# Kernel tuning notes

Hardware: AMD Instinct MI355X
Metric: run time of the kernel (lower is better)

## Reference

```python
import jax, jax.numpy as jnp
import numpy as np

B, S, D = 32, 200, 256          # batch, seq_len (hard-coded 200), emb_dim (hard-coded 256)
H_CLS, H_TNS, H = 2, 4, 6       # classical heads, tensor heads, total (rate=1/3, num_heads=6)
DFF, VOCAB, L, TD = 1024, 3500, 8, 2


def layer_norm(x, g, b, eps=1e-6):
    m = x.mean(-1, keepdims=True)
    v = ((x - m) ** 2).mean(-1, keepdims=True)
    return (x - m) * jax.lax.rsqrt(v + eps) * g + b


def setup_inputs() -> dict:
    key = jax.random.key(0)
    ks = jax.random.split(key, 12)
    n = jax.random.normal
    s1 = 1.0 / np.sqrt(4 + TD - 1.0)       # TNLayer RandomNormal stddev for A1/A4
    s2 = 1.0 / np.sqrt(4 + 2 * TD - 1.0)   # for A2/A3
    return {
        "tokens": jax.random.randint(ks[0], (B, S), 0, VOCAB),
        "tok_emb": n(ks[1], (VOCAB, D)) * 0.02,
        "pos_emb": n(ks[2], (S, D)) * 0.02,
        # stacked over L layers; axis 1 of size 3 is (q, k, v)
        "wqkv_w": n(ks[3], (L, 3, D, 2 * D)) * 0.05,
        "wqkv_b": jnp.zeros((L, 3, 2 * D)),
        "A1": n(ks[4], (L, 3, 4, TD, 4)) * s1,
        "A2": n(ks[5], (L, 3, 4, TD, TD, 8)) * s2,
        "A3": n(ks[6], (L, 3, 4, TD, TD, 8)) * s2,
        "A4": n(ks[7], (L, 3, 4, TD, 4)) * s1,
        "tnb": jnp.zeros((L, 3, 4 * D)),
        "out_w": n(ks[8], (L, H * D, D)) * 0.02,
        "out_b": jnp.zeros((L, D)),
        "ff1_w": n(ks[9], (L, D, DFF)) * 0.05,
        "ff1_b": jnp.zeros((L, DFF)),
        "ff2_w": n(ks[10], (L, DFF, D)) * 0.03,
        "ff2_b": jnp.zeros((L, D)),
        "ln1_g": jnp.ones((L, D)), "ln1_b": jnp.zeros((L, D)),
        "ln2_g": jnp.ones((L, D)), "ln2_b": jnp.zeros((L, D)),
    }


def bert_tensor_forward(tokens, tok_emb, pos_emb, wqkv_w, wqkv_b, A1, A2, A3, A4, tnb,
                        out_w, out_b, ff1_w, ff1_b, ff2_w, ff2_b, ln1_g, ln1_b, ln2_g, ln2_b):
    # embedding: positions array with start_index=1 is [0,1,...,199] -> pos_emb itself
    h = tok_emb[tokens] + pos_emb[None]                      # [B,S,D]
    # Attention_mask: 1.0 where token==0 (pad), broadcast over heads and query pos
    bias = (tokens == 0).astype(jnp.float32)[:, None, None, :] * (-1e9)  # [B,1,1,S]
    inv_sqrt_dk = 1.0 / jnp.sqrt(jnp.float32(D))

    def step(h, p):
        ww, wb, a1, a2, a3, a4, tb, ow, ob, f1w, f1b, f2w, f2b, g1, b1, g2, b2 = p
        # classical q/k/v heads: Dense(d_model * 2) -> [3,B,2,S,D]
        cls = jnp.einsum('bsd,xdf->xbsf', h, ww) + wb[:, None, None, :]
        cls = cls.reshape(3, B, S, H_CLS, D).transpose(0, 1, 3, 2, 4)
        # tensor-network q/k/v heads (TNLayer): MPO contraction over 4x4x4x4 split of D
        x6 = h.reshape(B, S, 4, 4, 4, 4)
        tns = jnp.einsum('bspqrt,xpmi,xqmnj,xrnok,xtol->xbsijkl', x6, a1, a2, a3, a4)
        tns = tns.reshape(3, B, S, 4 * D) + tb[:, None, None, :]
        tns = tns.reshape(3, B, S, H_TNS, D).transpose(0, 1, 3, 2, 4)  # [3,B,4,S,D]
        qkv = jnp.concatenate([cls, tns], axis=2)                      # [3,B,H,S,D]
        q, k, v = qkv[0], qkv[1], qkv[2]
        scores = jnp.einsum('bhqd,bhkd->bhqk', q, k) * inv_sqrt_dk + bias
        attn = jax.nn.softmax(scores, axis=-1)
        ctx = jnp.einsum('bhqk,bhkd->bhqd', attn, v)
        ctx = ctx.transpose(0, 2, 1, 3).reshape(B, S, H * D)           # [B,S,1536]
        out1 = layer_norm(h + ctx @ ow + ob, g1, b1)
        ffn = jax.nn.relu(out1 @ f1w + f1b) @ f2w + f2b
        return layer_norm(out1 + ffn, g2, b2), None

    xs = (wqkv_w, wqkv_b, A1, A2, A3, A4, tnb, out_w, out_b,
          ff1_w, ff1_b, ff2_w, ff2_b, ln1_g, ln1_b, ln2_g, ln2_b)
    h, _ = jax.lax.scan(step, h, xs)
    return h


def reference(tokens, tok_emb, pos_emb, wqkv_w, wqkv_b, A1, A2, A3, A4, tnb,
              out_w, out_b, ff1_w, ff1_b, ff2_w, ff2_b, ln1_g, ln1_b, ln2_g, ln2_b):
    return bert_tensor_forward(tokens, tok_emb, pos_emb, wqkv_w, wqkv_b, A1, A2, A3, A4,
                               tnb, out_w, out_b, ff1_w, ff1_b, ff2_w, ff2_b,
                               ln1_g, ln1_b, ln2_g, ln2_b)
```

## Files before the change

### kernel.cpp

```cpp
#include <hip/hip_runtime.h>
#include <hip/hip_bf16.h>

typedef __bf16 bf16x8 __attribute__((ext_vector_type(8)));
typedef float f32x4 __attribute__((ext_vector_type(4)));

#define NB 32
#define NS 200
#define SP 256
#define ND 256
#define NH 6
#define NL 8
#define NBS (NB*NS)
#define NZ (NB*NH)
#define SLAB (SP*ND)
#define PSTR 264

using bf16 = __hip_bfloat16;

enum { EPI_F32 = 0, EPI_RELU_BF = 1, EPI_QKV = 2, EPI_VT = 3 };

__device__ __forceinline__ float b2f(bf16 x) { return __bfloat162float(x); }
__device__ __forceinline__ bf16 f2b(float x) { return __float2bfloat16(x); }
__device__ __forceinline__ unsigned short fbits(float x) { bf16 h = f2b(x); return *(unsigned short*)&h; }

__device__ __forceinline__ void gload16(const bf16* g, const short* l) {
    __builtin_amdgcn_global_load_lds(
        (const __attribute__((address_space(1))) unsigned int*)(unsigned long long)(g),
        (__attribute__((address_space(3))) unsigned int*)(unsigned long long)(l), 16, 0, 0);
}

template<int MODE>
__global__ __launch_bounds__(256)
void gemm_nt(const bf16* __restrict__ A, const bf16* __restrict__ Bm,
             int M, int N, int K, int Kspan, long long sOz,
             float* __restrict__ outF, bf16* __restrict__ outBf,
             const float* __restrict__ bias,
             const float* __restrict__ qkvb, const float* __restrict__ tnbp,
             bf16* __restrict__ Qb, bf16* __restrict__ Kb, bf16* __restrict__ Vb)
{
    __shared__ short Asl[3][128*32];
    __shared__ short Bsl[3][128*32];
    const int tid  = threadIdx.x;
    const int m0   = blockIdx.y * 128;
    const int n0   = blockIdx.x * 128;
    const int kbase= blockIdx.z * Kspan;
    const int lane = tid & 63, w = tid >> 6;
    const int wm   = (w >> 1) * 64, wn = (w & 1) * 64;
    const int fr   = lane & 15, kc = (lane >> 4) * 8;
    const int srow = lane >> 2, schk = (lane & 3) * 8;

    const bf16* Ag = A  + (long long)m0 * K + kbase;
    const bf16* Bg = Bm + (long long)n0 * K + kbase;

    f32x4 acc[4][4];
#pragma unroll
    for (int i = 0; i < 4; i++)
#pragma unroll
        for (int j = 0; j < 4; j++) acc[i][j] = (f32x4){0.f,0.f,0.f,0.f};

    auto stage = [&](int buf, int k0) {
        gload16(Ag + (long long)(w*32      + srow)*K + k0 + schk, &Asl[buf][(w*32     )*32]);
        gload16(Ag + (long long)(w*32 + 16 + srow)*K + k0 + schk, &Asl[buf][(w*32 + 16)*32]);
        gload16(Bg + (long long)(w*32      + srow)*K + k0 + schk, &Bsl[buf][(w*32     )*32]);
        gload16(Bg + (long long)(w*32 + 16 + srow)*K + k0 + schk, &Bsl[buf][(w*32 + 16)*32]);
    };

    const int nt = Kspan >> 5;
    stage(0, 0);
    stage(1, 32);
    for (int t = 0; t < nt; t++) {
        const int buf = t % 3;
        if (t + 2 < nt) {
            stage((t + 2) % 3, (t + 2) * 32);
            asm volatile("s_waitcnt vmcnt(8)" ::: "memory");
        } else if (t + 1 < nt) {
            asm volatile("s_waitcnt vmcnt(4)" ::: "memory");
        } else {
            asm volatile("s_waitcnt vmcnt(0)" ::: "memory");
        }
        __builtin_amdgcn_s_barrier();
        __builtin_amdgcn_sched_barrier(0);
        bf16x8 af[4], bfm[4];
#pragma unroll
        for (int i = 0; i < 4; i++) af[i]  = *(const bf16x8*)&Asl[buf][(wm + i*16 + fr)*32 + kc];
#pragma unroll
        for (int j = 0; j < 4; j++) bfm[j] = *(const bf16x8*)&Bsl[buf][(wn + j*16 + fr)*32 + kc];
#pragma unroll
        for (int i = 0; i < 4; i++)
#pragma unroll
            for (int j = 0; j < 4; j++)
                acc[i][j] = __builtin_amdgcn_mfma_f32_16x16x32_bf16(af[i], bfm[j], acc[i][j], 0, 0, 0);
        __builtin_amdgcn_s_barrier();
        __builtin_amdgcn_sched_barrier(0);
    }

    const int rq = (lane >> 4) * 4;
#pragma unroll
    for (int i = 0; i < 4; i++) {
        const int r0 = m0 + wm + i*16 + rq;
        int b2r = 0, s20 = 0, hdV = 0, dd0 = 0;
        float bvv[4];
        if (MODE == EPI_QKV) { b2r = r0 / NS; s20 = r0 - b2r*NS; }
        if (MODE == EPI_VT) {
            hdV = r0 >> 8; dd0 = r0 & 255;
#pragma unroll
            for (int rg = 0; rg < 4; rg++) {
                const int rr = r0 + rg;
                bvv[rg] = (rr < 512) ? qkvb[1024 + rr] : tnbp[2048 + rr - 512];
            }
        }
#pragma unroll
        for (int j = 0; j < 4; j++) {
            const int c = n0 + wn + j*16 + fr;
            if (MODE == EPI_F32) {
#pragma unroll
                for (int rg = 0; rg < 4; rg++)
                    outF[(long long)blockIdx.z * sOz + (long long)(r0+rg)*N + c] = acc[i][j][rg];
            } else if (MODE == EPI_RELU_BF) {
                const float bv = bias[c];
#pragma unroll
                for (int rg = 0; rg < 4; rg++)
                    outBf[(long long)(r0+rg)*N + c] = f2b(fmaxf(acc[i][j][rg] + bv, 0.f));
            } else if (MODE == EPI_QKV) {
                const int x  = (c >= 1536);
                const int c1 = c - x*1536;
                const int hd = c1 >> 8, dd = c1 & 255;
                const float bv = (c1 < 512) ? qkvb[x*512 + c1] : tnbp[x*1024 + (c1 - 512)];
                bf16* dst = x ? Kb : Qb;
#pragma unroll
                for (int rg = 0; rg < 4; rg++) {
                    int bb = b2r, ss = s20 + rg;
                    if (ss >= NS) { bb++; ss -= NS; }
                    dst[((long long)((bb*NH + hd)*SP + ss))*ND + dd] = f2b(acc[i][j][rg] + bv);
                }
            } else {
                const int b2 = c / NS;
                const int s2 = c - b2*NS;
                const long long base = ((long long)((b2*NH + hdV)*ND + dd0))*SP + s2;
#pragma unroll
                for (int rg = 0; rg < 4; rg++)
                    Vb[base + (long long)rg*SP] = f2b(acc[i][j][rg] + bvv[rg]);
            }
        }
    }
}

__global__ __launch_bounds__(256)
void attn_fused(const bf16* __restrict__ Qb, const bf16* __restrict__ Kb,
                const bf16* __restrict__ Vtb, const int* __restrict__ tokens,
                bf16* __restrict__ ctx)
{
    __shared__ __align__(16) char smem[2*20480 + 1024 + 1024 + 64*PSTR*2];
    float* red   = (float*)(smem + 40960);
    float* maskv = (float*)(smem + 40960 + 1024);
    short* P     = (short*)(smem + 40960 + 2048);

    const int z  = blockIdx.x;
    const int b  = z / NH, h = z - b*NH;
    const int q0 = blockIdx.y * 64;
    const int tid = threadIdx.x;
    const int lane = tid & 63, w = tid >> 6;
    const int fr = lane & 15, qh = lane >> 4;
    const int kc = qh * 8;
    const int srow = lane >> 2, schk = (lane & 3) * 8;

    const bf16* Kp = Kb  + (long long)z * SLAB;
    const bf16* Qp = Qb  + (long long)z * SLAB;
    const bf16* Vp = Vtb + (long long)z * SLAB;

    {
        const int s = tid;
        float mv = -1e9f;
        if (s < NS && tokens[b*NS + s] != 0) mv = 0.f;
        maskv[s] = mv;
    }

    auto stage1 = [&](int buf, int k0) {
        short* Ks = (short*)(smem + buf*20480);
        short* Qs = (short*)(smem + buf*20480 + 16384);
#pragma unroll
        for (int r2 = 0; r2 < 4; r2++)
            gload16(Kp + (long long)(w*64 + r2*16 + srow)*ND + k0 + schk, &Ks[(w*64 + r2*16)*32]);
        gload16(Qp + (long long)(q0 + w*16 + srow)*ND + k0 + schk, &Qs[(w*16)*32]);
    };

    f32x4 acc[4][4];
#pragma unroll
    for (int i = 0; i < 4; i++)
#pragma unroll
        for (int j = 0; j < 4; j++) acc[i][j] = (f32x4){0.f,0.f,0.f,0.f};

    stage1(0, 0);
    for (int t = 0; t < 8; t++) {
        const int buf = t & 1;
        if (t + 1 < 8) {
            stage1(buf ^ 1, (t + 1) * 32);
            asm volatile("s_waitcnt vmcnt(5)" ::: "memory");
        } else {
            asm volatile("s_waitcnt vmcnt(0)" ::: "memory");
        }
        __builtin_amdgcn_s_barrier();
        __builtin_amdgcn_sched_barrier(0);
        const short* Ks = (const short*)(smem + buf*20480);
        const short* Qs = (const short*)(smem + buf*20480 + 16384);
        bf16x8 ak[4], bq[4];
#pragma unroll
        for (int i = 0; i < 4; i++) ak[i] = *(const bf16x8*)&Ks[(w*64 + i*16 + fr)*32 + kc];
#pragma unroll
        for (int j = 0; j < 4; j++) bq[j] = *(const bf16x8*)&Qs[(j*16 + fr)*32 + kc];
#pragma unroll
        for (int i = 0; i < 4; i++)
#pragma unroll
            for (int j = 0; j < 4; j++)
                acc[i][j] = __builtin_amdgcn_mfma_f32_16x16x32_bf16(ak[i], bq[j], acc[i][j], 0, 0, 0);
        __builtin_amdgcn_s_barrier();
        __builtin_amdgcn_sched_barrier(0);
    }

    float mk[4][4];
#pragma unroll
    for (int i = 0; i < 4; i++)
#pragma unroll
        for (int rg = 0; rg < 4; rg++) mk[i][rg] = maskv[w*64 + i*16 + qh*4 + rg];
#pragma unroll
    for (int i = 0; i < 4; i++)
#pragma unroll
        for (int j = 0; j < 4; j++)
#pragma unroll
            for (int rg = 0; rg < 4; rg++)
                acc[i][j][rg] = acc[i][j][rg] * 0.0625f + mk[i][rg];

    float pm[4];
#pragma unroll
    for (int j = 0; j < 4; j++) {
        float m = -3.0e38f;
#pragma unroll
        for (int i = 0; i < 4; i++)
#pragma unroll
            for (int rg = 0; rg < 4; rg++) m = fmaxf(m, acc[i][j][rg]);
        m = fmaxf(m, __shfl_xor(m, 16));
        m = fmaxf(m, __shfl_xor(m, 32));
        pm[j] = m;
    }
#pragma unroll
    for (int j = 0; j < 4; j++) red[w*64 + j*16 + fr] = pm[j];
    __syncthreads();
    float gm[4];
#pragma unroll
    for (int j = 0; j < 4; j++)
        gm[j] = fmaxf(fmaxf(red[j*16 + fr], red[64 + j*16 + fr]),
                      fmaxf(red[128 + j*16 + fr], red[192 + j*16 + fr]));
    float ps[4] = {0.f, 0.f, 0.f, 0.f};
#pragma unroll
    for (int i = 0; i < 4; i++)
#pragma unroll
        for (int j = 0; j < 4; j++)
#pragma unroll
            for (int rg = 0; rg < 4; rg++) {
                float e = __expf(acc[i][j][rg] - gm[j]);
                acc[i][j][rg] = e;
                ps[j] += e;
            }
#pragma unroll
    for (int j = 0; j < 4; j++) {
        ps[j] += __shfl_xor(ps[j], 16);
        ps[j] += __shfl_xor(ps[j], 32);
    }
    __syncthreads();
#pragma unroll
    for (int j = 0; j < 4; j++) red[w*64 + j*16 + fr] = ps[j];
    __syncthreads();
    float inv[4];
#pragma unroll
    for (int j = 0; j < 4; j++)
        inv[j] = 1.f / (red[j*16 + fr] + red[64 + j*16 + fr] + red[128 + j*16 + fr] + red[192 + j*16 + fr]);

#pragma unroll
    for (int i = 0; i < 4; i++)
#pragma unroll
        for (int j = 0; j < 4; j++) {
            ushort4 pk;
            pk.x = fbits(acc[i][j][0] * inv[j]);
            pk.y = fbits(acc[i][j][1] * inv[j]);
            pk.z = fbits(acc[i][j][2] * inv[j]);
            pk.w = fbits(acc[i][j][3] * inv[j]);
            *(ushort4*)&P[(j*16 + fr)*PSTR + w*64 + i*16 + qh*4] = pk;
        }
    __syncthreads();

    auto stage2 = [&](int buf, int s0) {
        short* Vs = (short*)(smem + buf*20480);
#pragma unroll
        for (int r2 = 0; r2 < 4; r2++)
            gload16(Vp + (long long)(w*64 + r2*16 + srow)*SP + s0 + schk, &Vs[(w*64 + r2*16)*32]);
    };

    f32x4 acc2[4][4];
#pragma unroll
    for (int i = 0; i < 4; i++)
#pragma unroll
        for (int j = 0; j < 4; j++) acc2[i][j] = (f32x4){0.f,0.f,0.f,0.f};

    stage2(0, 0);
    for (int t = 0; t < 7; t++) {
        const int buf = t & 1;
        if (t + 1 < 7) {
            stage2(buf ^ 1, (t + 1) * 32);
            asm volatile("s_waitcnt vmcnt(4)" ::: "memory");
        } else {
            asm volatile("s_waitcnt vmcnt(0)" ::: "memory");
        }
        __builtin_amdgcn_s_barrier();
        __builtin_amdgcn_sched_barrier(0);
        const short* Vs = (const short*)(smem + buf*20480);
        bf16x8 ap[4], bv[4];
#pragma unroll
        for (int i = 0; i < 4; i++) ap[i] = *(const bf16x8*)&P[(i*16 + fr)*PSTR + t*32 + kc];
#pragma unroll
        for (int j = 0; j < 4; j++) bv[j] = *(const bf16x8*)&Vs[(w*64 + j*16 + fr)*32 + kc];
#pragma unroll
        for (int i = 0; i < 4; i++)
#pragma unroll
            for (int j = 0; j < 4; j++)
                acc2[i][j] = __builtin_amdgcn_mfma_f32_16x16x32_bf16(ap[i], bv[j], acc2[i][j], 0, 0, 0);
        __builtin_amdgcn_s_barrier();
        __builtin_amdgcn_sched_barrier(0);
    }

#pragma unroll
    for (int i = 0; i < 4; i++)
#pragma unroll
        for (int j = 0; j < 4; j++)
#pragma unroll
            for (int rg = 0; rg < 4; rg++) {
                const int qg = q0 + i*16 + qh*4 + rg;
                if (qg < NS) {
                    const int d = w*64 + j*16 + fr;
                    ctx[((long long)(b*NS + qg))*1536 + h*256 + d] = f2b(acc2[i][j][rg]);
                }
            }
}

__global__ void embed_kernel(const int* __restrict__ tokens, const float* __restrict__ tok_emb,
                             const float* __restrict__ pos_emb, float* __restrict__ hf,
                             bf16* __restrict__ hbf)
{
    long long id = (long long)blockIdx.x * 256 + threadIdx.x;
    if (id >= (long long)NBS * ND) return;
    long long r = id >> 8;
    int j = id & 255;
    int tk = tokens[r];
    int s  = (int)(r % NS);
    float v = tok_emb[(long long)tk * ND + j] + pos_emb[s * ND + j];
    hf[id]  = v;
    hbf[id] = f2b(v);
}

__global__ void transpose_w(const float* __restrict__ in, bf16* __restrict__ out,
                            int L, int R, int C, long long total)
{
    long long id = (long long)blockIdx.x * 256 + threadIdx.x;
    if (id >= total) return;
    int l = (int)(id / ((long long)R * C));
    long long rem = id - (long long)l * R * C;
    int c = (int)(rem / R);
    int r = (int)(rem - (long long)c * R);
    out[id] = f2b(in[((long long)l * R + r) * C + c]);
}

__global__ void pack_cls(const float* __restrict__ wqkv, bf16* __restrict__ wcat)
{
    long long id = (long long)blockIdx.x * 256 + threadIdx.x;
    if (id >= 24ll * 512 * 256) return;
    int lx = (int)(id / (512 * 256));
    int rem = (int)(id - (long long)lx * 512 * 256);
    int n = rem >> 8;
    int k = rem & 255;
    wcat[((long long)lx * 1536 + n) * 256 + k] = f2b(wqkv[((long long)lx * 256 + k) * 512 + n]);
}

__global__ __launch_bounds__(256)
void build_wtns(const float* __restrict__ A1, const float* __restrict__ A2,
                const float* __restrict__ A3, const float* __restrict__ A4,
                bf16* __restrict__ wcat)
{
    int lx = blockIdx.x;
    __shared__ float a1s[32], a2s[128], a3s[128], a4s[32];
    int t = threadIdx.x;
    if (t < 32)  { a1s[t] = A1[lx*32 + t]; a4s[t] = A4[lx*32 + t]; }
    if (t < 128) { a2s[t] = A2[lx*128 + t]; a3s[t] = A3[lx*128 + t]; }
    __syncthreads();
    int d = t;
    int p = d >> 6, q = (d >> 4) & 3, rr = (d >> 2) & 3, tt = d & 3;
    for (int i = 0; i < 4; i++) {
        float w1_0 = a1s[(p*2 + 0)*4 + i];
        float w1_1 = a1s[(p*2 + 1)*4 + i];
        for (int j = 0; j < 8; j++) {
            float c1_0 = w1_0 * a2s[((q*2+0)*2+0)*8 + j] + w1_1 * a2s[((q*2+1)*2+0)*8 + j];
            float c1_1 = w1_0 * a2s[((q*2+0)*2+1)*8 + j] + w1_1 * a2s[((q*2+1)*2+1)*8 + j];
            for (int kk = 0; kk < 8; kk++) {
                float c2_0 = c1_0 * a3s[((rr*2+0)*2+0)*8 + kk] + c1_1 * a3s[((rr*2+1)*2+0)*8 + kk];
                float c2_1 = c1_0 * a3s[((rr*2+0)*2+1)*8 + kk] + c1_1 * a3s[((rr*2+1)*2+1)*8 + kk];
                for (int ll = 0; ll < 4; ll++) {
                    float sv = c2_0 * a4s[(tt*2 + 0)*4 + ll] + c2_1 * a4s[(tt*2 + 1)*4 + ll];
                    int e = ((i*8 + j)*8 + kk)*4 + ll;
                    wcat[((long long)lx * 1536 + 512 + e) * 256 + d] = f2b(sv);
                }
            }
        }
    }
}

__global__ __launch_bounds__(256)
void ln_kernel(const float* __restrict__ raw0, const float* __restrict__ raw1,
               const float* __restrict__ bias, const float* __restrict__ resid,
               const float* __restrict__ g, const float* __restrict__ bb,
               float* __restrict__ outF, bf16* __restrict__ outBf)
{
    int w = threadIdx.x >> 6, lane = threadIdx.x & 63;
    long long r = (long long)blockIdx.x * 4 + w;
    long long base = r * ND;
    float x[4]; float s = 0.f;
#pragma unroll
    for (int c = 0; c < 4; c++) {
        int j = lane + 64*c;
        x[c] = resid[base + j] + raw0[base + j] + raw1[base + j] + bias[j];
        s += x[c];
    }
#pragma unroll
    for (int o = 32; o; o >>= 1) s += __shfl_xor(s, o);
    float mean = s * (1.f/256.f);
    float vs = 0.f;
#pragma unroll
    for (int c = 0; c < 4; c++) { float d = x[c] - mean; vs += d*d; }
#pragma unroll
    for (int o = 32; o; o >>= 1) vs += __shfl_xor(vs, o);
    float rs = rsqrtf(vs * (1.f/256.f) + 1e-6f);
#pragma unroll
    for (int c = 0; c < 4; c++) {
        int j = lane + 64*c;
        float y = (x[c] - mean) * rs * g[j] + bb[j];
        outF[base + j]  = y;
        outBf[base + j] = f2b(y);
    }
}

extern "C" void kernel_launch(void* const* d_in, const int* in_sizes, int n_in,
                              void* d_out, int out_size, void* d_ws, size_t ws_size,
                              hipStream_t stream)
{
    const int*   tokens  = (const int*)  d_in[0];
    const float* tok_emb = (const float*)d_in[1];
    const float* pos_emb = (const float*)d_in[2];
    const float* wqkv_w  = (const float*)d_in[3];
    const float* wqkv_b  = (const float*)d_in[4];
    const float* A1      = (const float*)d_in[5];
    const float* A2      = (const float*)d_in[6];
    const float* A3      = (const float*)d_in[7];
    const float* A4      = (const float*)d_in[8];
    const float* tnb     = (const float*)d_in[9];
    const float* out_w   = (const float*)d_in[10];
    const float* out_b   = (const float*)d_in[11];
    const float* ff1_w   = (const float*)d_in[12];
    const float* ff1_b   = (const float*)d_in[13];
    const float* ff2_w   = (const float*)d_in[14];
    const float* ff2_b   = (const float*)d_in[15];
    const float* ln1_g   = (const float*)d_in[16];
    const float* ln1_b   = (const float*)d_in[17];
    const float* ln2_g   = (const float*)d_in[18];
    const float* ln2_b   = (const float*)d_in[19];

    char* ws = (char*)d_ws;
    size_t off = 0;
    auto alloc = [&](size_t bytes) -> char* {
        char* p = ws + off;
        off += (bytes + 255) & ~(size_t)255;
        return p;
    };
    float* hf    = (float*)alloc((size_t)NBS * ND * 4);
    bf16*  hbf   = (bf16*) alloc((size_t)NBS * ND * 2);
    bf16*  wcat  = (bf16*) alloc(24ull * 1536 * 256 * 2);
    bf16*  owt   = (bf16*) alloc(8ull * 256 * 1536 * 2);
    bf16*  f1wt  = (bf16*) alloc(8ull * 1024 * 256 * 2);
    bf16*  f2wt  = (bf16*) alloc(8ull * 256 * 1024 * 2);
    bf16*  Qb    = (bf16*) alloc((size_t)NZ * SLAB * 2);
    bf16*  Kb    = (bf16*) alloc((size_t)NZ * SLAB * 2);
    bf16*  Vtb   = (bf16*) alloc((size_t)NZ * SLAB * 2);
    bf16*  ctxg  = (bf16*) alloc((size_t)NBS * 1536 * 2);
    bf16*  ffn   = (bf16*) alloc((size_t)NBS * 1024 * 2);
    float* raw   = (float*)alloc((size_t)NBS * ND * 4 * 2);
    float* out1f = (float*)alloc((size_t)NBS * ND * 4);
    bf16*  out1bf= (bf16*) alloc((size_t)NBS * ND * 2);
    if (off > ws_size) return;
    float* raw1 = raw + (size_t)NBS * ND;

    hipMemsetAsync(Qb,  0, (size_t)NZ * SLAB * 2, stream);
    hipMemsetAsync(Kb,  0, (size_t)NZ * SLAB * 2, stream);
    hipMemsetAsync(Vtb, 0, (size_t)NZ * SLAB * 2, stream);

    embed_kernel<<<NBS, 256, 0, stream>>>(tokens, tok_emb, pos_emb, hf, hbf);
    pack_cls<<<12288, 256, 0, stream>>>(wqkv_w, wcat);
    build_wtns<<<24, 256, 0, stream>>>(A1, A2, A3, A4, wcat);
    transpose_w<<<12288, 256, 0, stream>>>(out_w, owt, 8, 1536, 256, 8ll*1536*256);
    transpose_w<<<8192, 256, 0, stream>>>(ff1_w, f1wt, 8, 256, 1024, 8ll*256*1024);
    transpose_w<<<8192, 256, 0, stream>>>(ff2_w, f2wt, 8, 1024, 256, 8ll*1024*256);

    for (int l = 0; l < NL; l++) {
        const bf16* wl = wcat + (long long)l * 3 * 1536 * 256;
        gemm_nt<EPI_QKV><<<dim3(24, 50, 1), 256, 0, stream>>>(
            hbf, wl, NBS, 3072, 256, 256, 0, nullptr, nullptr, nullptr,
            wqkv_b + l * 3 * 512, tnb + l * 3 * 1024, Qb, Kb, nullptr);
        gemm_nt<EPI_VT><<<dim3(50, 12, 1), 256, 0, stream>>>(
            wl + 2ll * 1536 * 256, hbf, 1536, NBS, 256, 256, 0, nullptr, nullptr, nullptr,
            wqkv_b + l * 3 * 512, tnb + l * 3 * 1024, nullptr, nullptr, Vtb);
        attn_fused<<<dim3(NZ, 4), 256, 0, stream>>>(Qb, Kb, Vtb, tokens, ctxg);
        gemm_nt<EPI_F32><<<dim3(2, 50, 2), 256, 0, stream>>>(
            ctxg, owt + (long long)l * 256 * 1536, NBS, 256, 1536, 768, (long long)NBS*ND,
            raw, nullptr, nullptr, nullptr, nullptr, nullptr, nullptr, nullptr);
        ln_kernel<<<1600, 256, 0, stream>>>(raw, raw1, out_b + l * 256, hf,
                                            ln1_g + l * 256, ln1_b + l * 256, out1f, out1bf);
        gemm_nt<EPI_RELU_BF><<<dim3(8, 50, 1), 256, 0, stream>>>(
            out1bf, f1wt + (long long)l * 1024 * 256, NBS, 1024, 256, 256, 0,
            nullptr, ffn, ff1_b + l * 1024, nullptr, nullptr, nullptr, nullptr, nullptr);
        gemm_nt<EPI_F32><<<dim3(2, 50, 2), 256, 0, stream>>>(
            ffn, f2wt + (long long)l * 256 * 1024, NBS, 256, 1024, 512, (long long)NBS*ND,
            raw, nullptr, nullptr, nullptr, nullptr, nullptr, nullptr, nullptr);
        ln_kernel<<<1600, 256, 0, stream>>>(raw, raw1, ff2_b + l * 256, out1f,
                                            ln2_g + l * 256, ln2_b + l * 256,
                                            (l == NL - 1) ? (float*)d_out : hf, hbf);
    }
}
```

Before: 1.046 ms.

## Merge Q/K/V projections into one transposed GEMM and tile weight transposes

Replaces the separate Q/K projection GEMM and V-transposed GEMM with a single GEMM that computes the weights times activations for all 4608 output features. Its epilogue routes Q/K rows with packed 4-element stores and V rows to the transposed layout. The weight preprocessing transposes now go through a shared-memory tiled kernel instead of strided per-element gathers, and the three memsets are folded into one, which assumes Qb, Kb and Vtb are contiguous. This saves a launch and speeds up one-time preprocessing, at the cost of Q/K stores now being strided across the sequence dimension.

```diff
diff --git a/kernel.cpp b/kernel.cpp
--- a/kernel.cpp
+++ b/kernel.cpp
@@ -17,7 +17,7 @@
 
 using bf16 = __hip_bfloat16;
 
-enum { EPI_F32 = 0, EPI_RELU_BF = 1, EPI_QKV = 2, EPI_VT = 3 };
+enum { EPI_F32 = 0, EPI_RELU_BF = 1, EPI_QKVT = 2 };
 
 __device__ __forceinline__ float b2f(bf16 x) { return __bfloat162float(x); }
 __device__ __forceinline__ bf16 f2b(float x) { return __float2bfloat16(x); }
@@ -98,15 +98,16 @@
 #pragma unroll
     for (int i = 0; i < 4; i++) {
         const int r0 = m0 + wm + i*16 + rq;
-        int b2r = 0, s20 = 0, hdV = 0, dd0 = 0;
+        int xq = 0, hdq = 0, dd0 = 0;
         float bvv[4];
-        if (MODE == EPI_QKV) { b2r = r0 / NS; s20 = r0 - b2r*NS; }
-        if (MODE == EPI_VT) {
-            hdV = r0 >> 8; dd0 = r0 & 255;
+        if (MODE == EPI_QKVT) {
+            xq  = r0 / 1536;
+            const int c1 = r0 - xq*1536;
+            hdq = c1 >> 8; dd0 = c1 & 255;
 #pragma unroll
             for (int rg = 0; rg < 4; rg++) {
-                const int rr = r0 + rg;
-                bvv[rg] = (rr < 512) ? qkvb[1024 + rr] : tnbp[2048 + rr - 512];
+                const int cc = c1 + rg;
+                bvv[rg] = (cc < 512) ? qkvb[xq*512 + cc] : tnbp[xq*1024 + cc - 512];
             }
         }
 #pragma unroll
@@ -121,25 +122,23 @@
 #pragma unroll
                 for (int rg = 0; rg < 4; rg++)
                     outBf[(long long)(r0+rg)*N + c] = f2b(fmaxf(acc[i][j][rg] + bv, 0.f));
-            } else if (MODE == EPI_QKV) {
-                const int x  = (c >= 1536);
-                const int c1 = c - x*1536;
-                const int hd = c1 >> 8, dd = c1 & 255;
-                const float bv = (c1 < 512) ? qkvb[x*512 + c1] : tnbp[x*1024 + (c1 - 512)];
-                bf16* dst = x ? Kb : Qb;
-#pragma unroll
-                for (int rg = 0; rg < 4; rg++) {
-                    int bb = b2r, ss = s20 + rg;
-                    if (ss >= NS) { bb++; ss -= NS; }
-                    dst[((long long)((bb*NH + hd)*SP + ss))*ND + dd] = f2b(acc[i][j][rg] + bv);
+            } else {
+                const int bb = c / NS;
+                const int ss = c - bb*NS;
+                if (xq == 2) {
+                    const long long base = ((long long)((bb*NH + hdq)*ND + dd0))*SP + ss;
+#pragma unroll
+                    for (int rg = 0; rg < 4; rg++)
+                        Vb[base + (long long)rg*SP] = f2b(acc[i][j][rg] + bvv[rg]);
+                } else {
+                    bf16* dst = xq ? Kb : Qb;
+                    ushort4 pk;
+                    pk.x = fbits(acc[i][j][0] + bvv[0]);
+                    pk.y = fbits(acc[i][j][1] + bvv[1]);
+                    pk.z = fbits(acc[i][j][2] + bvv[2]);
+                    pk.w = fbits(acc[i][j][3] + bvv[3]);
+                    *(ushort4*)&dst[((long long)((bb*NH + hdq)*SP + ss))*ND + dd0] = pk;
                 }
-            } else {
-                const int b2 = c / NS;
-                const int s2 = c - b2*NS;
-                const long long base = ((long long)((b2*NH + hdV)*ND + dd0))*SP + s2;
-#pragma unroll
-                for (int rg = 0; rg < 4; rg++)
-                    Vb[base + (long long)rg*SP] = f2b(acc[i][j][rg] + bvv[rg]);
             }
         }
     }
@@ -356,27 +355,27 @@
     hbf[id] = f2b(v);
 }
 
-__global__ void transpose_w(const float* __restrict__ in, bf16* __restrict__ out,
-                            int L, int R, int C, long long total)
-{
-    long long id = (long long)blockIdx.x * 256 + threadIdx.x;
-    if (id >= total) return;
-    int l = (int)(id / ((long long)R * C));
-    long long rem = id - (long long)l * R * C;
-    int c = (int)(rem / R);
-    int r = (int)(rem - (long long)c * R);
-    out[id] = f2b(in[((long long)l * R + r) * C + c]);
-}
-
-__global__ void pack_cls(const float* __restrict__ wqkv, bf16* __restrict__ wcat)
-{
-    long long id = (long long)blockIdx.x * 256 + threadIdx.x;
-    if (id >= 24ll * 512 * 256) return;
-    int lx = (int)(id / (512 * 256));
-    int rem = (int)(id - (long long)lx * 512 * 256);
-    int n = rem >> 8;
-    int k = rem & 255;
-    wcat[((long long)lx * 1536 + n) * 256 + k] = f2b(wqkv[((long long)lx * 256 + k) * 512 + n]);
+__global__ __launch_bounds__(256)
+void transpose_tile(const float* __restrict__ in, bf16* __restrict__ out,
+                    int R, int C, long long inL, long long outL, int outStride)
+{
+    __shared__ float tl[32][33];
+    const int l  = blockIdx.z;
+    const int r0 = blockIdx.y * 32, c0 = blockIdx.x * 32;
+    const float* ip = in + (long long)l * inL;
+    bf16* op = out + (long long)l * outL;
+    const int tx = threadIdx.x & 31, ty = threadIdx.x >> 5;
+#pragma unroll
+    for (int i = 0; i < 4; i++) {
+        const int r = r0 + ty + i*8;
+        tl[ty + i*8][tx] = ip[(long long)r * C + c0 + tx];
+    }
+    __syncthreads();
+#pragma unroll
+    for (int i = 0; i < 4; i++) {
+        const int c = c0 + ty + i*8;
+        op[(long long)c * outStride + r0 + tx] = f2b(tl[tx][ty + i*8]);
+    }
 }
 
 __global__ __launch_bounds__(256)
@@ -494,25 +493,24 @@
     if (off > ws_size) return;
     float* raw1 = raw + (size_t)NBS * ND;
 
-    hipMemsetAsync(Qb,  0, (size_t)NZ * SLAB * 2, stream);
-    hipMemsetAsync(Kb,  0, (size_t)NZ * SLAB * 2, stream);
-    hipMemsetAsync(Vtb, 0, (size_t)NZ * SLAB * 2, stream);
+    hipMemsetAsync(Qb, 0, (size_t)3 * NZ * SLAB * 2, stream);
 
     embed_kernel<<<NBS, 256, 0, stream>>>(tokens, tok_emb, pos_emb, hf, hbf);
-    pack_cls<<<12288, 256, 0, stream>>>(wqkv_w, wcat);
+    transpose_tile<<<dim3(16, 8, 24), 256, 0, stream>>>(
+        wqkv_w, wcat, 256, 512, 256ll*512, 1536ll*256, 256);
     build_wtns<<<24, 256, 0, stream>>>(A1, A2, A3, A4, wcat);
-    transpose_w<<<12288, 256, 0, stream>>>(out_w, owt, 8, 1536, 256, 8ll*1536*256);
-    transpose_w<<<8192, 256, 0, stream>>>(ff1_w, f1wt, 8, 256, 1024, 8ll*256*1024);
-    transpose_w<<<8192, 256, 0, stream>>>(ff2_w, f2wt, 8, 1024, 256, 8ll*1024*256);
+    transpose_tile<<<dim3(8, 48, 8), 256, 0, stream>>>(
+        out_w, owt, 1536, 256, 1536ll*256, 256ll*1536, 1536);
+    transpose_tile<<<dim3(32, 8, 8), 256, 0, stream>>>(
+        ff1_w, f1wt, 256, 1024, 256ll*1024, 1024ll*256, 256);
+    transpose_tile<<<dim3(8, 32, 8), 256, 0, stream>>>(
+        ff2_w, f2wt, 1024, 256, 1024ll*256, 256ll*1024, 1024);
 
     for (int l = 0; l < NL; l++) {
         const bf16* wl = wcat + (long long)l * 3 * 1536 * 256;
-        gemm_nt<EPI_QKV><<<dim3(24, 50, 1), 256, 0, stream>>>(
-            hbf, wl, NBS, 3072, 256, 256, 0, nullptr, nullptr, nullptr,
-            wqkv_b + l * 3 * 512, tnb + l * 3 * 1024, Qb, Kb, nullptr);
-        gemm_nt<EPI_VT><<<dim3(50, 12, 1), 256, 0, stream>>>(
-            wl + 2ll * 1536 * 256, hbf, 1536, NBS, 256, 256, 0, nullptr, nullptr, nullptr,
-            wqkv_b + l * 3 * 512, tnb + l * 3 * 1024, nullptr, nullptr, Vtb);
+        gemm_nt<EPI_QKVT><<<dim3(50, 36, 1), 256, 0, stream>>>(
+            wl, hbf, 4608, NBS, 256, 256, 0, nullptr, nullptr, nullptr,
+            wqkv_b + l * 3 * 512, tnb + l * 3 * 1024, Qb, Kb, Vtb);
         attn_fused<<<dim3(NZ, 4), 256, 0, stream>>>(Qb, Kb, Vtb, tokens, ctxg);
         gemm_nt<EPI_F32><<<dim3(2, 50, 2), 256, 0, stream>>>(
             ctxg, owt + (long long)l * 256 * 1536, NBS, 256, 1536, 768, (long long)NBS*ND,
```

Measured after the change: 1.019 ms. 2.5% less time.
